# Kernel tuning notes

Hardware: AMD Instinct MI355X
Metric: run time of the kernel (lower is better)

The kernel has to match this reference:

```python
import jax, jax.numpy as jnp
import numpy as np

B, L, H, Z, T = 128, 4096, 1024, 256, 16  # batch, input_len(64*64), lstm_hidden, z_size, timesteps


def _lstm_cell(x, h, c, W_ih, b_ih, W_hh, b_hh):
    # PyTorch LSTMCell: gates ordered (input, forget, cell, output)
    gates = x @ W_ih.T + b_ih + h @ W_hh.T + b_hh
    i, f, g, o = jnp.split(gates, 4, axis=-1)
    c_new = jax.nn.sigmoid(f) * c + jax.nn.sigmoid(i) * jnp.tanh(g)
    h_new = jax.nn.sigmoid(o) * jnp.tanh(c_new)
    return h_new, c_new


def setup_inputs() -> dict:
    key = jax.random.key(0)
    ks = jax.random.split(key, 16)
    s = 0.02  # weight init scale
    return {
        "x": jax.random.uniform(ks[0], (B, L), dtype=jnp.float32),
        "eps": jax.random.normal(ks[1], (T, B, Z), dtype=jnp.float32),
        "c_0": jax.random.normal(ks[2], (1, L), dtype=jnp.float32),
        "h_0_enc": jax.random.normal(ks[3], (H,), dtype=jnp.float32),
        "h_0_dec": jax.random.normal(ks[4], (H,), dtype=jnp.float32),
        "W_ih_enc": jax.random.normal(ks[5], (4 * H, 2 * L + H), dtype=jnp.float32) * s,
        "b_ih_enc": jnp.zeros((4 * H,), dtype=jnp.float32),
        "W_hh_enc": jax.random.normal(ks[6], (4 * H, H), dtype=jnp.float32) * s,
        "b_hh_enc": jnp.zeros((4 * H,), dtype=jnp.float32),
        "W_mu": jax.random.normal(ks[7], (Z, H), dtype=jnp.float32) * s,
        "b_mu": jnp.zeros((Z,), dtype=jnp.float32),
        "W_sigma": jax.random.normal(ks[8], (Z, H), dtype=jnp.float32) * s,
        "b_sigma": jnp.zeros((Z,), dtype=jnp.float32),
        "W_ih_dec": jax.random.normal(ks[9], (4 * H, Z), dtype=jnp.float32) * s,
        "b_ih_dec": jnp.zeros((4 * H,), dtype=jnp.float32),
        "W_hh_dec": jax.random.normal(ks[10], (4 * H, H), dtype=jnp.float32) * s,
        "b_hh_dec": jnp.zeros((4 * H,), dtype=jnp.float32),
        "W_write": jax.random.normal(ks[11], (L, H), dtype=jnp.float32) * s,
        "b_write": jnp.zeros((L,), dtype=jnp.float32),
    }


def reference(x, eps, c_0, h_0_enc, h_0_dec,
              W_ih_enc, b_ih_enc, W_hh_enc, b_hh_enc,
              W_mu, b_mu, W_sigma, b_sigma,
              W_ih_dec, b_ih_dec, W_hh_dec, b_hh_dec,
              W_write, b_write):
    batch = x.shape[0]
    c_t = jnp.broadcast_to(c_0, (batch, L))
    h_enc = jnp.broadcast_to(h_0_enc, (batch, H))
    h_dec = jnp.broadcast_to(h_0_dec, (batch, H))
    c_enc = jnp.zeros((batch, H), dtype=x.dtype)
    c_dec = jnp.zeros((batch, H), dtype=x.dtype)

    def step(carry, eps_t):
        c_t, h_enc, c_enc, h_dec, c_dec = carry
        x_hat = x - jax.nn.sigmoid(c_t)
        r_t = jnp.concatenate((x, x_hat, h_dec), axis=-1)  # read + concat with h_dec
        h_enc, c_enc = _lstm_cell(r_t, h_enc, c_enc, W_ih_enc, b_ih_enc, W_hh_enc, b_hh_enc)
        mu = h_enc @ W_mu.T + b_mu
        logsigma = h_enc @ W_sigma.T + b_sigma
        z_t = eps_t * jnp.exp(logsigma) + mu
        h_dec, c_dec = _lstm_cell(z_t, h_dec, c_dec, W_ih_dec, b_ih_dec, W_hh_dec, b_hh_dec)
        c_t = c_t + h_dec @ W_write.T + b_write
        return (c_t, h_enc, c_enc, h_dec, c_dec), None

    (c_t, _, _, _, _), _ = jax.lax.scan(step, (c_t, h_enc, c_enc, h_dec, c_dec), eps)
    return jax.nn.sigmoid(c_t)
```

## Files before the change

### kernel.cpp

```cpp
#include <hip/hip_runtime.h>

#define B_   128
#define T_   16

typedef __bf16 bf16;
typedef __bf16 bf16x4 __attribute__((ext_vector_type(4)));
typedef __bf16 bf16x8 __attribute__((ext_vector_type(8)));
typedef float f32x4 __attribute__((ext_vector_type(4)));

#define GLL(SRC, DST) __builtin_amdgcn_global_load_lds( \
    (const __attribute__((address_space(1))) void*)(SRC), \
    (__attribute__((address_space(3))) void*)(DST), 16, 0, 0)

#define MFMA __builtin_amdgcn_mfma_f32_16x16x32_bf16
#define SLICE 524288

__device__ __forceinline__ float sigf(float x) { return 1.f / (1.f + expf(-x)); }

__device__ __forceinline__ void core64(
    bf16 (&As)[2][4096], bf16 (&Bs)[2][4096],
    const bf16* __restrict__ Ab, int lda,
    const bf16* __restrict__ Wb, int ldw,
    int nk, f32x4 (&acc)[4])
{
    const int tid = threadIdx.x, lane = tid & 63, wave = tid >> 6;
    const int srow = lane >> 3;
    const int scol = ((lane & 7) ^ srow) << 3;
    const int wr = wave & 1, wc = wave >> 1;
    const int ln = lane & 15;
    const int rA0 = wr * 32 + ln;
    const int rB0 = wc * 32 + ln;
    const int swz = (lane & 7) << 4;
    const int kq  = (lane >> 4) << 4;

    auto stage = [&](int b, int koff) {
        int c0 = wave, c1 = wave + 4;
        int ra0 = c0 * 8 + srow, ra1 = c1 * 8 + srow;
        GLL(Ab + (size_t)ra0 * lda + koff + scol, &As[b][c0 * 512]);
        GLL(Ab + (size_t)ra1 * lda + koff + scol, &As[b][c1 * 512]);
        GLL(Wb + (size_t)ra0 * ldw + koff + scol, &Bs[b][c0 * 512]);
        GLL(Wb + (size_t)ra1 * ldw + koff + scol, &Bs[b][c1 * 512]);
    };

    stage(0, 0);
    int bq = 0;
    for (int it = 0; it < nk; ++it) {
        __syncthreads();
        if (it + 1 < nk) stage(bq ^ 1, (it + 1) << 6);
        const bf16* as = As[bq];
        const bf16* bs = Bs[bq];
#pragma unroll
        for (int k2 = 0; k2 < 2; ++k2) {
            const int co = (((k2 << 6) | kq) ^ swz) >> 1;
            bf16x8 a0 = *(const bf16x8*)&as[rA0 * 64 + co];
            bf16x8 a1 = *(const bf16x8*)&as[(rA0 + 16) * 64 + co];
            bf16x8 b0 = *(const bf16x8*)&bs[rB0 * 64 + co];
            bf16x8 b1 = *(const bf16x8*)&bs[(rB0 + 16) * 64 + co];
            acc[0] = MFMA(a0, b0, acc[0], 0, 0, 0);
            acc[1] = MFMA(a0, b1, acc[1], 0, 0, 0);
            acc[2] = MFMA(a1, b0, acc[2], 0, 0, 0);
            acc[3] = MFMA(a1, b1, acc[3], 0, 0, 0);
        }
        bq ^= 1;
    }
}

__device__ __forceinline__ void store64f(float* __restrict__ P, int bm, int bn,
                                         f32x4 (&acc)[4])
{
    const int lane = threadIdx.x & 63, wave = threadIdx.x >> 6;
    const int wr = wave & 1, wc = wave >> 1;
    const int ln = lane & 15, q = lane >> 4;
    const int row0 = bm + wr * 32 + q * 4;
    const int col0 = bn + wc * 32 + ln;
#pragma unroll
    for (int r = 0; r < 4; ++r) {
        P[(size_t)(row0 + r) * 4096 + col0]           = acc[0][r];
        P[(size_t)(row0 + r) * 4096 + col0 + 16]      = acc[1][r];
        P[(size_t)(row0 + 16 + r) * 4096 + col0]      = acc[2][r];
        P[(size_t)(row0 + 16 + r) * 4096 + col0 + 16] = acc[3][r];
    }
}

__device__ __forceinline__ void store64b(bf16* __restrict__ P, int bm, int bn,
                                         f32x4 (&acc)[4])
{
    const int lane = threadIdx.x & 63, wave = threadIdx.x >> 6;
    const int wr = wave & 1, wc = wave >> 1;
    const int ln = lane & 15, q = lane >> 4;
    const int row0 = bm + wr * 32 + q * 4;
    const int col0 = bn + wc * 32 + ln;
#pragma unroll
    for (int r = 0; r < 4; ++r) {
        P[(size_t)(row0 + r) * 4096 + col0]           = (bf16)acc[0][r];
        P[(size_t)(row0 + r) * 4096 + col0 + 16]      = (bf16)acc[1][r];
        P[(size_t)(row0 + 16 + r) * 4096 + col0]      = (bf16)acc[2][r];
        P[(size_t)(row0 + 16 + r) * 4096 + col0 + 16] = (bf16)acc[3][r];
    }
}

__global__ __launch_bounds__(256) void gemm64_k(
    const bf16* __restrict__ A, int lda,
    const bf16* __restrict__ W, int ldw, int Kc,
    float* __restrict__ P)
{
    __shared__ bf16 As[2][4096], Bs[2][4096];
    const int nt = blockIdx.x, mt = blockIdx.y, zz = blockIdx.z;
    f32x4 acc[4];
#pragma unroll
    for (int i = 0; i < 4; ++i) acc[i] = (f32x4){0.f, 0.f, 0.f, 0.f};
    const bf16* Ab = A + (size_t)mt * 64 * lda + (size_t)zz * Kc;
    const bf16* Wb = W + (size_t)nt * 64 * ldw + (size_t)zz * Kc;
    core64(As, Bs, Ab, lda, Wb, ldw, Kc >> 6, acc);
    store64f(P + (size_t)zz * SLICE, mt * 64, nt * 64, acc);
}

__global__ __launch_bounds__(256) void gemm64b_k(
    const bf16* __restrict__ A, int lda,
    const bf16* __restrict__ W, int ldw, int Kc,
    bf16* __restrict__ P)
{
    __shared__ bf16 As[2][4096], Bs[2][4096];
    const int nt = blockIdx.x, mt = blockIdx.y, zz = blockIdx.z;
    f32x4 acc[4];
#pragma unroll
    for (int i = 0; i < 4; ++i) acc[i] = (f32x4){0.f, 0.f, 0.f, 0.f};
    const bf16* Ab = A + (size_t)mt * 64 * lda + (size_t)zz * Kc;
    const bf16* Wb = W + (size_t)nt * 64 * ldw + (size_t)zz * Kc;
    core64(As, Bs, Ab, lda, Wb, ldw, Kc >> 6, acc);
    store64b(P + (size_t)zz * SLICE, mt * 64, nt * 64, acc);
}

__global__ __launch_bounds__(256) void kE_k(
    const bf16* __restrict__ hh,   const bf16* __restrict__ Wwr,
    const bf16* __restrict__ Wcat, const bf16* __restrict__ Wdh,
    bf16* __restrict__ wrP, bf16* __restrict__ encP, bf16* __restrict__ decP,
    int zoff)
{
    __shared__ bf16 As[2][4096], Bs[2][4096];
    const int nt = blockIdx.x, mt = blockIdx.y, zz = blockIdx.z + zoff;
    f32x4 acc[4];
#pragma unroll
    for (int i = 0; i < 4; ++i) acc[i] = (f32x4){0.f, 0.f, 0.f, 0.f};

    const bf16* Ab;
    const bf16* Wb;
    int ldw;
    bf16* P;
    if (zz < 2) {
        Ab = hh + (size_t)mt * 64 * 2048 + zz * 512;
        Wb = Wwr + (size_t)nt * 64 * 1024 + zz * 512;
        ldw = 1024; P = wrP + (size_t)zz * SLICE;
    } else if (zz < 6) {
        int s = zz - 2;
        Ab = hh + (size_t)mt * 64 * 2048 + s * 512;
        Wb = Wcat + (size_t)nt * 64 * 2048 + s * 512;
        ldw = 2048; P = encP + (size_t)(8 + s) * SLICE;
    } else {
        int g = zz - 6;
        Ab = hh + (size_t)mt * 64 * 2048 + g * 512;
        Wb = Wdh + (size_t)nt * 64 * 1024 + g * 512;
        ldw = 1024; P = decP + (size_t)g * SLICE;
    }
    core64(As, Bs, Ab, 2048, Wb, ldw, 8, acc);
    store64b(P, mt * 64, nt * 64, acc);
}

__global__ __launch_bounds__(256) void fin0_k(
    const float* __restrict__ P, float* __restrict__ base,
    const float* __restrict__ b1, const float* __restrict__ b2)
{
    const int i = blockIdx.x * 256 + threadIdx.x;
    const int row = i >> 10, j = i & 1023;
    const size_t off = (size_t)row * 4096 + (j << 2);
    float s0 = 0.f, s1 = 0.f, s2 = 0.f, s3 = 0.f;
#pragma unroll
    for (int z = 0; z < 4; ++z) {
        float4 p = *(const float4*)(P + (size_t)z * SLICE + off);
        s0 += p.x; s1 += p.y; s2 += p.z; s3 += p.w;
    }
    base[off + 0] = s0 + b1[j]        + b2[j];
    base[off + 1] = s1 + b1[1024 + j] + b2[1024 + j];
    base[off + 2] = s2 + b1[2048 + j] + b2[2048 + j];
    base[off + 3] = s3 + b1[3072 + j] + b2[3072 + j];
}

__global__ __launch_bounds__(256) void kB_k(
    const bf16* __restrict__ encP, const float* __restrict__ base,
    float* __restrict__ c_enc, bf16* __restrict__ hh)
{
    const int i = blockIdx.x * 256 + threadIdx.x;
    const int row = i >> 10, j = i & 1023;
    const size_t off = (size_t)row * 4096 + (j << 2);
    float s0 = 0.f, s1 = 0.f, s2 = 0.f, s3 = 0.f;
#pragma unroll
    for (int z = 0; z < 12; ++z) {
        bf16x4 p = *(const bf16x4*)(encP + (size_t)z * SLICE + off);
        s0 += (float)p[0]; s1 += (float)p[1]; s2 += (float)p[2]; s3 += (float)p[3];
    }
    float4 bb = *(const float4*)(base + off);
    float gi = s0 + bb.x, gf = s1 + bb.y, gg = s2 + bb.z, go = s3 + bb.w;
    float cn = sigf(gf) * c_enc[i] + sigf(gi) * tanhf(gg);
    c_enc[i] = cn;
    hh[(size_t)row * 2048 + 1024 + j] = (bf16)(sigf(go) * tanhf(cn));
}

__global__ __launch_bounds__(256) void kF_k(
    const bf16* __restrict__ wrP, const float* __restrict__ b_wr,
    float* __restrict__ c_t, bf16* __restrict__ negs, float* __restrict__ outp)
{
    const int qi = blockIdx.x * 256 + threadIdx.x;
    const int row = qi >> 10, cq = qi & 1023;
    const size_t off = (size_t)row * 4096 + (cq << 2);
    bf16x4 p0 = *(const bf16x4*)(wrP + off);
    bf16x4 p1 = *(const bf16x4*)(wrP + SLICE + off);
    float4 cv = *(const float4*)(c_t + off);
    float4 bw = *(const float4*)(b_wr + (cq << 2));
    float v0 = cv.x + (float)p0[0] + (float)p1[0] + bw.x;
    float v1 = cv.y + (float)p0[1] + (float)p1[1] + bw.y;
    float v2 = cv.z + (float)p0[2] + (float)p1[2] + bw.z;
    float v3 = cv.w + (float)p0[3] + (float)p1[3] + bw.w;
    *(float4*)(c_t + off) = make_float4(v0, v1, v2, v3);
    negs[off + 0] = (bf16)(-sigf(v0));
    negs[off + 1] = (bf16)(-sigf(v1));
    negs[off + 2] = (bf16)(-sigf(v2));
    negs[off + 3] = (bf16)(-sigf(v3));
    if (outp)
        *(float4*)(outp + off) = make_float4(sigf(v0), sigf(v1), sigf(v2), sigf(v3));
}

struct SmemG32 {
    bf16 As[4][128][64];
    bf16 Ws[4][32][64];
};

__global__ __launch_bounds__(256) void kC_k(
    const bf16* __restrict__ hh, const bf16* __restrict__ Wms,
    const float* __restrict__ b_mu, const float* __restrict__ b_sig,
    const float* __restrict__ eps_t, bf16* __restrict__ zbf)
{
    __shared__ SmemG32 sm;
    const int nt = blockIdx.x;
    const int tid = threadIdx.x, lane = tid & 63, wave = tid >> 6;
    const int srow = lane >> 3, scol = ((lane & 7) ^ srow) << 3;
    const int ln = lane & 15, kq = (lane >> 4) << 4;
    const int swz = (lane & 7) << 4;
    const int rA = wave * 32 + ln;
    const bf16* Wb = Wms + (size_t)nt * 32 * 1024;
    const bf16* Ab = hh + 1024;

    f32x4 acc[2][2];
#pragma unroll
    for (int m = 0; m < 2; ++m)
#pragma unroll
        for (int n = 0; n < 2; ++n) acc[m][n] = (f32x4){0.f, 0.f, 0.f, 0.f};

    for (int it = 0; it < 4; ++it) {
        if (it) __syncthreads();
        const int koff = it * 256;
#pragma unroll
        for (int kc = 0; kc < 4; ++kc) {
            const int kg = koff + kc * 64 + scol;
#pragma unroll
            for (int i = 0; i < 4; ++i) {
                int rb = i * 32 + wave * 8;
                GLL(Ab + (size_t)(rb + srow) * 2048 + kg, &sm.As[kc][rb][0]);
            }
            GLL(Wb + (size_t)(wave * 8 + srow) * 1024 + kg, &sm.Ws[kc][wave * 8][0]);
        }
        __syncthreads();
#pragma unroll
        for (int kc = 0; kc < 4; ++kc)
#pragma unroll
            for (int k2 = 0; k2 < 2; ++k2) {
                const int co = (((k2 << 6) | kq) ^ swz) >> 1;
                bf16x8 a0 = *(const bf16x8*)&sm.As[kc][rA][co];
                bf16x8 a1 = *(const bf16x8*)&sm.As[kc][rA + 16][co];
                bf16x8 b0 = *(const bf16x8*)&sm.Ws[kc][ln][co];
                bf16x8 b1 = *(const bf16x8*)&sm.Ws[kc][ln + 16][co];
                acc[0][0] = MFMA(a0, b0, acc[0][0], 0, 0, 0);
                acc[0][1] = MFMA(a0, b1, acc[0][1], 0, 0, 0);
                acc[1][0] = MFMA(a1, b0, acc[1][0], 0, 0, 0);
                acc[1][1] = MFMA(a1, b1, acc[1][1], 0, 0, 0);
            }
    }
    __syncthreads();

    float* Cl = (float*)&sm;
    const int q = lane >> 4;
#pragma unroll
    for (int f = 0; f < 2; ++f)
#pragma unroll
        for (int n = 0; n < 2; ++n)
#pragma unroll
            for (int r = 0; r < 4; ++r)
                Cl[(wave * 32 + f * 16 + q * 4 + r) * 33 + n * 16 + ln] = acc[f][n][r];
    __syncthreads();

#pragma unroll
    for (int it = 0; it < 8; ++it) {
        int li = it * 256 + tid;
        int row = li >> 4, zl = li & 15;
        int zi = nt * 16 + zl;
        float mu = Cl[row * 33 + zl * 2]     + b_mu[zi];
        float ls = Cl[row * 33 + zl * 2 + 1] + b_sig[zi];
        float z = eps_t[row * 256 + zi] * expf(ls) + mu;
        zbf[(size_t)row * 256 + zi] = (bf16)z;
    }
}

struct SmemD {
    bf16 As[4][128][64];
    bf16 Ws[4][64][64];
};

__global__ __launch_bounds__(256) void kD_k(
    const bf16* __restrict__ zbf, const bf16* __restrict__ Wdz,
    const bf16* __restrict__ decP,
    const float* __restrict__ b_ihd, const float* __restrict__ b_hhd,
    float* __restrict__ c_dec, bf16* __restrict__ hh)
{
    __shared__ SmemD sm;
    const int nt = blockIdx.x;
    const int tid = threadIdx.x, lane = tid & 63, wave = tid >> 6;
    const int srow = lane >> 3, scol = ((lane & 7) ^ srow) << 3;
    const int ln = lane & 15, q = lane >> 4;
    const int kq = q << 4, swz = (lane & 7) << 4;
    const int wr = wave & 1, wc = wave >> 1;
    const bf16* Wb = Wdz + (size_t)nt * 64 * 256;

    f32x4 acc[4][2];
#pragma unroll
    for (int f = 0; f < 4; ++f)
#pragma unroll
        for (int n = 0; n < 2; ++n) acc[f][n] = (f32x4){0.f, 0.f, 0.f, 0.f};

#pragma unroll
    for (int kc = 0; kc < 4; ++kc) {
        const int kg = kc * 64 + scol;
#pragma unroll
        for (int i = 0; i < 4; ++i) {
            int rb = i * 32 + wave * 8;
            GLL(zbf + (size_t)(rb + srow) * 256 + kg, &sm.As[kc][rb][0]);
        }
#pragma unroll
        for (int i = 0; i < 2; ++i) {
            int rbw = i * 32 + wave * 8;
            GLL(Wb + (size_t)(rbw + srow) * 256 + kg, &sm.Ws[kc][rbw][0]);
        }
    }
    __syncthreads();
#pragma unroll
    for (int kc = 0; kc < 4; ++kc)
#pragma unroll
        for (int k2 = 0; k2 < 2; ++k2) {
            const int co = (((k2 << 6) | kq) ^ swz) >> 1;
            bf16x8 b0 = *(const bf16x8*)&sm.Ws[kc][wc * 32 + ln][co];
            bf16x8 b1 = *(const bf16x8*)&sm.Ws[kc][wc * 32 + ln + 16][co];
#pragma unroll
            for (int f = 0; f < 4; ++f) {
                bf16x8 a = *(const bf16x8*)&sm.As[kc][wr * 64 + f * 16 + ln][co];
                acc[f][0] = MFMA(a, b0, acc[f][0], 0, 0, 0);
                acc[f][1] = MFMA(a, b1, acc[f][1], 0, 0, 0);
            }
        }
    __syncthreads();

    float* Cl = (float*)&sm;
#pragma unroll
    for (int f = 0; f < 4; ++f)
#pragma unroll
        for (int n = 0; n < 2; ++n)
#pragma unroll
            for (int r = 0; r < 4; ++r)
                Cl[(wr * 64 + f * 16 + q * 4 + r) * 66 + wc * 32 + n * 16 + ln] = acc[f][n][r];
    __syncthreads();

#pragma unroll
    for (int it = 0; it < 8; ++it) {
        int li = it * 256 + tid;
        int row = li >> 4, jl = li & 15;
        int J = nt * 16 + jl;
        const float* cr = &Cl[row * 66 + jl * 4];
        int gcol = nt * 64 + jl * 4;
        const bf16* gp = decP + (size_t)row * 4096 + gcol;
        bf16x4 g0v = *(const bf16x4*)gp;
        bf16x4 g1v = *(const bf16x4*)(gp + SLICE);
        float gi = cr[0] + (float)g0v[0] + (float)g1v[0] + b_ihd[J]        + b_hhd[J];
        float gf = cr[1] + (float)g0v[1] + (float)g1v[1] + b_ihd[1024 + J] + b_hhd[1024 + J];
        float gg = cr[2] + (float)g0v[2] + (float)g1v[2] + b_ihd[2048 + J] + b_hhd[2048 + J];
        float go = cr[3] + (float)g0v[3] + (float)g1v[3] + b_ihd[3072 + J] + b_hhd[3072 + J];
        int ci = row * 1024 + J;
        float cn = sigf(gf) * c_dec[ci] + sigf(gi) * tanhf(gg);
        c_dec[ci] = cn;
        hh[(size_t)row * 2048 + J] = (bf16)(sigf(go) * tanhf(cn));
    }
}

#define PBL (B_ * 4096)
#define PBH (B_ * 1024)

__global__ void init_k(const float* __restrict__ x, const float* __restrict__ c0,
                       const float* __restrict__ h0e, const float* __restrict__ h0d,
                       float* __restrict__ c_t, float* __restrict__ c_enc,
                       float* __restrict__ c_dec, bf16* __restrict__ negs,
                       bf16* __restrict__ hh, bf16* __restrict__ x_bf) {
    int i = blockIdx.x * 256 + threadIdx.x;
    if (i >= PBL) return;
    int n = i & 4095;
    float c = c0[n];
    c_t[i] = c;
    negs[i] = (bf16)(-sigf(c));
    x_bf[i] = (bf16)x[i];
    if (i < PBH) {
        int row = i >> 10, j = i & 1023;
        c_enc[i] = 0.f;
        c_dec[i] = 0.f;
        hh[(size_t)row * 2048 + j]        = (bf16)h0d[j];
        hh[(size_t)row * 2048 + 1024 + j] = (bf16)h0e[j];
    }
}

__device__ __forceinline__ bf16x8 cvt8(const float* s) {
    float4 a = *(const float4*)s, b = *(const float4*)(s + 4);
    bf16x8 v = { (bf16)a.x, (bf16)a.y, (bf16)a.z, (bf16)a.w,
                 (bf16)b.x, (bf16)b.y, (bf16)b.z, (bf16)b.w };
    return v;
}

__global__ void conv_es_k(const float* __restrict__ Wih, const float* __restrict__ Whh,
                          bf16* __restrict__ wxh, bf16* __restrict__ wsum,
                          bf16* __restrict__ wcat) {
    int id = blockIdx.x * 256 + threadIdx.x;
    if (id >= 4096 * 768) return;
    int np = id / 768, c = (id - np * 768) * 8;
    int n = ((np & 3) << 10) + (np >> 2);
    if (c < 4096) {
        const float* sx = Wih + (size_t)n * 9216 + c;
        const float* sh = sx + 4096;
        float4 a = *(const float4*)sh, b = *(const float4*)(sh + 4);
        float4 e = *(const float4*)sx, f = *(const float4*)(sx + 4);
        bf16x8 vh = { (bf16)a.x, (bf16)a.y, (bf16)a.z, (bf16)a.w,
                      (bf16)b.x, (bf16)b.y, (bf16)b.z, (bf16)b.w };
        bf16x8 vs = { (bf16)(a.x + e.x), (bf16)(a.y + e.y), (bf16)(a.z + e.z), (bf16)(a.w + e.w),
                      (bf16)(b.x + f.x), (bf16)(b.y + f.y), (bf16)(b.z + f.z), (bf16)(b.w + f.w) };
        *(bf16x8*)(wxh  + (size_t)np * 4096 + c) = vh;
        *(bf16x8*)(wsum + (size_t)np * 4096 + c) = vs;
    } else if (c < 5120) {
        *(bf16x8*)(wcat + (size_t)np * 2048 + (c - 4096)) =
            cvt8(Wih + (size_t)n * 9216 + 8192 + (c - 4096));
    } else {
        *(bf16x8*)(wcat + (size_t)np * 2048 + 1024 + (c - 5120)) =
            cvt8(Whh + (size_t)n * 1024 + (c - 5120));
    }
}

__global__ void conv_dec_k(const float* __restrict__ Wih, const float* __restrict__ Whh,
                           bf16* __restrict__ wdz, bf16* __restrict__ wdh) {
    int id = blockIdx.x * 256 + threadIdx.x;
    if (id >= 4096 * 160) return;
    int np = id / 160, c = (id - np * 160) * 8;
    int n = ((np & 3) << 10) + (np >> 2);
    if (c < 256)
        *(bf16x8*)(wdz + (size_t)np * 256 + c) = cvt8(Wih + (size_t)n * 256 + c);
    else
        *(bf16x8*)(wdh + (size_t)np * 1024 + (c - 256)) =
            cvt8(Whh + (size_t)n * 1024 + (c - 256));
}

__global__ void conv_ms_k(const float* __restrict__ Wmu, const float* __restrict__ Wsig,
                          bf16* __restrict__ dst) {
    int id = blockIdx.x * 256 + threadIdx.x;
    if (id >= 512 * 128) return;
    int np = id >> 7, c = (id & 127) * 8;
    int zi = np >> 1;
    const float* src = ((np & 1) ? Wsig : Wmu) + (size_t)zi * 1024 + c;
    *(bf16x8*)(dst + (size_t)np * 1024 + c) = cvt8(src);
}

__global__ void conv_wr_k(const float* __restrict__ Wwr, bf16* __restrict__ dst) {
    int id = blockIdx.x * 256 + threadIdx.x;
    if (id >= 4096 * 128) return;
    *(bf16x8*)(dst + (size_t)id * 8) = cvt8(Wwr + (size_t)id * 8);
}

extern "C" void kernel_launch(void* const* d_in, const int* in_sizes, int n_in,
                              void* d_out, int out_size, void* d_ws, size_t ws_size,
                              hipStream_t stream) {
    const float* x      = (const float*)d_in[0];
    const float* eps    = (const float*)d_in[1];
    const float* c0     = (const float*)d_in[2];
    const float* h0e    = (const float*)d_in[3];
    const float* h0d    = (const float*)d_in[4];
    const float* W_ih_e = (const float*)d_in[5];
    const float* b_ih_e = (const float*)d_in[6];
    const float* W_hh_e = (const float*)d_in[7];
    const float* b_hh_e = (const float*)d_in[8];
    const float* W_mu   = (const float*)d_in[9];
    const float* b_mu   = (const float*)d_in[10];
    const float* W_sig  = (const float*)d_in[11];
    const float* b_sig  = (const float*)d_in[12];
    const float* W_ih_d = (const float*)d_in[13];
    const float* b_ih_d = (const float*)d_in[14];
    const float* W_hh_d = (const float*)d_in[15];
    const float* b_hh_d = (const float*)d_in[16];
    const float* W_wr   = (const float*)d_in[17];
    const float* b_wr   = (const float*)d_in[18];
    float* out = (float*)d_out;

    float* f = (float*)d_ws;
    float* c_t   = f; f += SLICE;
    float* base  = f; f += SLICE;
    float* pP    = f; f += (size_t)4 * SLICE;
    float* c_enc = f; f += 131072;
    float* c_dec = f; f += 131072;
    bf16* bp    = (bf16*)f;
    bf16* encP  = bp; bp += (size_t)12 * SLICE;
    bf16* decP  = bp; bp += (size_t)2 * SLICE;
    bf16* wrP   = bp; bp += (size_t)2 * SLICE;
    bf16* negs  = bp; bp += (size_t)B_ * 4096;
    bf16* hh    = bp; bp += (size_t)B_ * 2048;
    bf16* zbf   = bp; bp += (size_t)B_ * 256;
    bf16* x_bf  = bp; bp += (size_t)B_ * 4096;
    bf16* Wxh   = bp; bp += (size_t)4096 * 4096;
    bf16* Wsum  = bp; bp += (size_t)4096 * 4096;
    bf16* Wcat  = bp; bp += (size_t)4096 * 2048;
    bf16* Wdz   = bp; bp += (size_t)4096 * 256;
    bf16* Wdh   = bp; bp += (size_t)4096 * 1024;
    bf16* Wms   = bp; bp += (size_t)512 * 1024;
    bf16* Wwr   = bp; bp += (size_t)4096 * 1024;

    dim3 blk(256);

    init_k<<<(PBL + 255) / 256, blk, 0, stream>>>(x, c0, h0e, h0d, c_t, c_enc, c_dec,
                                                  negs, hh, x_bf);
    conv_es_k<<<(4096 * 768 + 255) / 256, blk, 0, stream>>>(W_ih_e, W_hh_e,
                                                            Wxh, Wsum, Wcat);
    conv_dec_k<<<(4096 * 160 + 255) / 256, blk, 0, stream>>>(W_ih_d, W_hh_d, Wdz, Wdh);
    conv_ms_k<<<(512 * 128 + 255) / 256, blk, 0, stream>>>(W_mu, W_sig, Wms);
    conv_wr_k<<<(4096 * 128 + 255) / 256, blk, 0, stream>>>(W_wr, Wwr);

    gemm64_k<<<dim3(64, 2, 4), blk, 0, stream>>>(x_bf, 4096, Wsum, 4096, 1024, pP);
    fin0_k<<<dim3(512), blk, 0, stream>>>(pP, base, b_ih_e, b_hh_e);

    kE_k<<<dim3(64, 2, 6), blk, 0, stream>>>(hh, Wwr, Wcat, Wdh, wrP, encP, decP, 2);

    for (int t = 0; t < T_; ++t) {
        gemm64b_k<<<dim3(64, 2, 8), blk, 0, stream>>>(negs, 4096, Wxh, 4096, 512, encP);
        kB_k<<<dim3(512), blk, 0, stream>>>(encP, base, c_enc, hh);
        kC_k<<<dim3(16), blk, 0, stream>>>(hh, Wms, b_mu, b_sig,
                                           eps + (size_t)t * (B_ * 256), zbf);
        kD_k<<<dim3(64), blk, 0, stream>>>(zbf, Wdz, decP, b_ih_d, b_hh_d, c_dec, hh);
        kE_k<<<dim3(64, 2, 8), blk, 0, stream>>>(hh, Wwr, Wcat, Wdh, wrP, encP, decP, 0);
        kF_k<<<dim3(512), blk, 0, stream>>>(wrP, b_wr, c_t, negs,
                                            (t == T_ - 1) ? out : nullptr);
    }
}
```

Measured before the change: 840.6 us.

## Merge prologue conversions, widen kB loads, and split kD across batch halves

Five separate weight-conversion and init kernels become one prolog kernel that dispatches on block index, which cuts launch overhead. kB now has each thread handle two hidden units with 16-byte bf16x8 loads over half as many blocks. kD is split into 128 blocks, each covering 64 batch rows, and reuses the shared core64 GEMM routine instead of its own custom load and MFMA loop. This raises parallelism in the small decoder GEMM but leaves each block with less work and possibly different pipelining.

```diff
diff --git a/kernel.cpp b/kernel.cpp
--- a/kernel.cpp
+++ b/kernel.cpp
@@ -190,19 +190,32 @@
     float* __restrict__ c_enc, bf16* __restrict__ hh)
 {
     const int i = blockIdx.x * 256 + threadIdx.x;
-    const int row = i >> 10, j = i & 1023;
-    const size_t off = (size_t)row * 4096 + (j << 2);
-    float s0 = 0.f, s1 = 0.f, s2 = 0.f, s3 = 0.f;
+    const int row = i >> 9, li = i & 511;
+    const size_t off = (size_t)row * 4096 + (li << 3);
+    float s[8] = {0.f, 0.f, 0.f, 0.f, 0.f, 0.f, 0.f, 0.f};
 #pragma unroll
     for (int z = 0; z < 12; ++z) {
-        bf16x4 p = *(const bf16x4*)(encP + (size_t)z * SLICE + off);
-        s0 += (float)p[0]; s1 += (float)p[1]; s2 += (float)p[2]; s3 += (float)p[3];
-    }
-    float4 bb = *(const float4*)(base + off);
-    float gi = s0 + bb.x, gf = s1 + bb.y, gg = s2 + bb.z, go = s3 + bb.w;
-    float cn = sigf(gf) * c_enc[i] + sigf(gi) * tanhf(gg);
-    c_enc[i] = cn;
-    hh[(size_t)row * 2048 + 1024 + j] = (bf16)(sigf(go) * tanhf(cn));
+        bf16x8 p = *(const bf16x8*)(encP + (size_t)z * SLICE + off);
+#pragma unroll
+        for (int k = 0; k < 8; ++k) s[k] += (float)p[k];
+    }
+    float4 bb0 = *(const float4*)(base + off);
+    float4 bb1 = *(const float4*)(base + off + 4);
+    const int j0 = li << 1;
+    {
+        float gi = s[0] + bb0.x, gf = s[1] + bb0.y, gg = s[2] + bb0.z, go = s[3] + bb0.w;
+        int ci = row * 1024 + j0;
+        float cn = sigf(gf) * c_enc[ci] + sigf(gi) * tanhf(gg);
+        c_enc[ci] = cn;
+        hh[(size_t)row * 2048 + 1024 + j0] = (bf16)(sigf(go) * tanhf(cn));
+    }
+    {
+        float gi = s[4] + bb1.x, gf = s[5] + bb1.y, gg = s[6] + bb1.z, go = s[7] + bb1.w;
+        int ci = row * 1024 + j0 + 1;
+        float cn = sigf(gf) * c_enc[ci] + sigf(gi) * tanhf(gg);
+        c_enc[ci] = cn;
+        hh[(size_t)row * 2048 + 1024 + j0 + 1] = (bf16)(sigf(go) * tanhf(cn));
+    }
 }
 
 __global__ __launch_bounds__(256) void kF_k(
@@ -309,10 +322,7 @@
     }
 }
 
-struct SmemD {
-    bf16 As[4][128][64];
-    bf16 Ws[4][64][64];
-};
+struct SmemK { bf16 A[2][4096]; bf16 B[2][4096]; };
 
 __global__ __launch_bounds__(256) void kD_k(
     const bf16* __restrict__ zbf, const bf16* __restrict__ Wdz,
@@ -320,70 +330,42 @@
     const float* __restrict__ b_ihd, const float* __restrict__ b_hhd,
     float* __restrict__ c_dec, bf16* __restrict__ hh)
 {
-    __shared__ SmemD sm;
-    const int nt = blockIdx.x;
+    __shared__ SmemK sm;
+    const int bid = blockIdx.x;
+    const int mt = bid & 1, nt = bid >> 1;
     const int tid = threadIdx.x, lane = tid & 63, wave = tid >> 6;
-    const int srow = lane >> 3, scol = ((lane & 7) ^ srow) << 3;
+    const int wr = wave & 1, wc = wave >> 1;
     const int ln = lane & 15, q = lane >> 4;
-    const int kq = q << 4, swz = (lane & 7) << 4;
-    const int wr = wave & 1, wc = wave >> 1;
+
+    const bf16* Ab = zbf + (size_t)mt * 64 * 256;
     const bf16* Wb = Wdz + (size_t)nt * 64 * 256;
-
-    f32x4 acc[4][2];
-#pragma unroll
-    for (int f = 0; f < 4; ++f)
-#pragma unroll
-        for (int n = 0; n < 2; ++n) acc[f][n] = (f32x4){0.f, 0.f, 0.f, 0.f};
-
-#pragma unroll
-    for (int kc = 0; kc < 4; ++kc) {
-        const int kg = kc * 64 + scol;
-#pragma unroll
-        for (int i = 0; i < 4; ++i) {
-            int rb = i * 32 + wave * 8;
-            GLL(zbf + (size_t)(rb + srow) * 256 + kg, &sm.As[kc][rb][0]);
-        }
-#pragma unroll
-        for (int i = 0; i < 2; ++i) {
-            int rbw = i * 32 + wave * 8;
-            GLL(Wb + (size_t)(rbw + srow) * 256 + kg, &sm.Ws[kc][rbw][0]);
-        }
-    }
+    f32x4 acc[4];
+#pragma unroll
+    for (int i = 0; i < 4; ++i) acc[i] = (f32x4){0.f, 0.f, 0.f, 0.f};
+    core64(sm.A, sm.B, Ab, 256, Wb, 256, 4, acc);
+
     __syncthreads();
-#pragma unroll
-    for (int kc = 0; kc < 4; ++kc)
-#pragma unroll
-        for (int k2 = 0; k2 < 2; ++k2) {
-            const int co = (((k2 << 6) | kq) ^ swz) >> 1;
-            bf16x8 b0 = *(const bf16x8*)&sm.Ws[kc][wc * 32 + ln][co];
-            bf16x8 b1 = *(const bf16x8*)&sm.Ws[kc][wc * 32 + ln + 16][co];
-#pragma unroll
-            for (int f = 0; f < 4; ++f) {
-                bf16x8 a = *(const bf16x8*)&sm.As[kc][wr * 64 + f * 16 + ln][co];
-                acc[f][0] = MFMA(a, b0, acc[f][0], 0, 0, 0);
-                acc[f][1] = MFMA(a, b1, acc[f][1], 0, 0, 0);
-            }
-        }
+    float* Cl = (float*)&sm;
+    const int r0 = wr * 32 + q * 4;
+    const int c0 = wc * 32 + ln;
+#pragma unroll
+    for (int r = 0; r < 4; ++r) {
+        Cl[(r0 + r) * 66 + c0]           = acc[0][r];
+        Cl[(r0 + r) * 66 + c0 + 16]      = acc[1][r];
+        Cl[(r0 + 16 + r) * 66 + c0]      = acc[2][r];
+        Cl[(r0 + 16 + r) * 66 + c0 + 16] = acc[3][r];
+    }
     __syncthreads();
 
-    float* Cl = (float*)&sm;
-#pragma unroll
-    for (int f = 0; f < 4; ++f)
-#pragma unroll
-        for (int n = 0; n < 2; ++n)
-#pragma unroll
-            for (int r = 0; r < 4; ++r)
-                Cl[(wr * 64 + f * 16 + q * 4 + r) * 66 + wc * 32 + n * 16 + ln] = acc[f][n][r];
-    __syncthreads();
-
-#pragma unroll
-    for (int it = 0; it < 8; ++it) {
+#pragma unroll
+    for (int it = 0; it < 4; ++it) {
         int li = it * 256 + tid;
-        int row = li >> 4, jl = li & 15;
-        int J = nt * 16 + jl;
-        const float* cr = &Cl[row * 66 + jl * 4];
-        int gcol = nt * 64 + jl * 4;
-        const bf16* gp = decP + (size_t)row * 4096 + gcol;
+        int lrow = li >> 4, jl = li & 15;
+        int row = mt * 64 + lrow;
+        int np0 = nt * 64 + jl * 4;
+        int J = np0 >> 2;
+        const float* cr = &Cl[lrow * 66 + jl * 4];
+        const bf16* gp = decP + (size_t)row * 4096 + np0;
         bf16x4 g0v = *(const bf16x4*)gp;
         bf16x4 g1v = *(const bf16x4*)(gp + SLICE);
         float gi = cr[0] + (float)g0v[0] + (float)g1v[0] + b_ihd[J]        + b_hhd[J];
@@ -400,13 +382,76 @@
 #define PBL (B_ * 4096)
 #define PBH (B_ * 1024)
 
-__global__ void init_k(const float* __restrict__ x, const float* __restrict__ c0,
-                       const float* __restrict__ h0e, const float* __restrict__ h0d,
-                       float* __restrict__ c_t, float* __restrict__ c_enc,
-                       float* __restrict__ c_dec, bf16* __restrict__ negs,
-                       bf16* __restrict__ hh, bf16* __restrict__ x_bf) {
-    int i = blockIdx.x * 256 + threadIdx.x;
-    if (i >= PBL) return;
+__device__ __forceinline__ bf16x8 cvt8(const float* s) {
+    float4 a = *(const float4*)s, b = *(const float4*)(s + 4);
+    bf16x8 v = { (bf16)a.x, (bf16)a.y, (bf16)a.z, (bf16)a.w,
+                 (bf16)b.x, (bf16)b.y, (bf16)b.z, (bf16)b.w };
+    return v;
+}
+
+__global__ __launch_bounds__(256) void prolog_k(
+    const float* __restrict__ x, const float* __restrict__ c0,
+    const float* __restrict__ h0e, const float* __restrict__ h0d,
+    const float* __restrict__ Wih_e, const float* __restrict__ Whh_e,
+    const float* __restrict__ Wih_d, const float* __restrict__ Whh_d,
+    const float* __restrict__ Wmu, const float* __restrict__ Wsig,
+    const float* __restrict__ Wwr_f,
+    float* __restrict__ c_t, float* __restrict__ c_enc, float* __restrict__ c_dec,
+    bf16* __restrict__ negs, bf16* __restrict__ hh, bf16* __restrict__ x_bf,
+    bf16* __restrict__ wxh, bf16* __restrict__ wsum, bf16* __restrict__ wcat,
+    bf16* __restrict__ wdz, bf16* __restrict__ wdh, bf16* __restrict__ wms,
+    bf16* __restrict__ wwr)
+{
+    const int bid = blockIdx.x;
+    if (bid < 12288) {
+        int id = bid * 256 + threadIdx.x;
+        int np = id / 768, c = (id - np * 768) * 8;
+        int n = ((np & 3) << 10) + (np >> 2);
+        if (c < 4096) {
+            const float* sx = Wih_e + (size_t)n * 9216 + c;
+            const float* sh = sx + 4096;
+            float4 a = *(const float4*)sh, b = *(const float4*)(sh + 4);
+            float4 e = *(const float4*)sx, f = *(const float4*)(sx + 4);
+            bf16x8 vh = { (bf16)a.x, (bf16)a.y, (bf16)a.z, (bf16)a.w,
+                          (bf16)b.x, (bf16)b.y, (bf16)b.z, (bf16)b.w };
+            bf16x8 vs = { (bf16)(a.x + e.x), (bf16)(a.y + e.y), (bf16)(a.z + e.z), (bf16)(a.w + e.w),
+                          (bf16)(b.x + f.x), (bf16)(b.y + f.y), (bf16)(b.z + f.z), (bf16)(b.w + f.w) };
+            *(bf16x8*)(wxh  + (size_t)np * 4096 + c) = vh;
+            *(bf16x8*)(wsum + (size_t)np * 4096 + c) = vs;
+        } else if (c < 5120) {
+            *(bf16x8*)(wcat + (size_t)np * 2048 + (c - 4096)) =
+                cvt8(Wih_e + (size_t)n * 9216 + 8192 + (c - 4096));
+        } else {
+            *(bf16x8*)(wcat + (size_t)np * 2048 + 1024 + (c - 5120)) =
+                cvt8(Whh_e + (size_t)n * 1024 + (c - 5120));
+        }
+        return;
+    }
+    if (bid < 12288 + 2560) {
+        int id = (bid - 12288) * 256 + threadIdx.x;
+        int np = id / 160, c = (id - np * 160) * 8;
+        int n = ((np & 3) << 10) + (np >> 2);
+        if (c < 256)
+            *(bf16x8*)(wdz + (size_t)np * 256 + c) = cvt8(Wih_d + (size_t)n * 256 + c);
+        else
+            *(bf16x8*)(wdh + (size_t)np * 1024 + (c - 256)) =
+                cvt8(Whh_d + (size_t)n * 1024 + (c - 256));
+        return;
+    }
+    if (bid < 12288 + 2560 + 256) {
+        int id = (bid - 12288 - 2560) * 256 + threadIdx.x;
+        int np = id >> 7, c = (id & 127) * 8;
+        int zi = np >> 1;
+        const float* src = ((np & 1) ? Wsig : Wmu) + (size_t)zi * 1024 + c;
+        *(bf16x8*)(wms + (size_t)np * 1024 + c) = cvt8(src);
+        return;
+    }
+    if (bid < 12288 + 2560 + 256 + 2048) {
+        int id = (bid - 12288 - 2560 - 256) * 256 + threadIdx.x;
+        *(bf16x8*)(wwr + (size_t)id * 8) = cvt8(Wwr_f + (size_t)id * 8);
+        return;
+    }
+    int i = (bid - 12288 - 2560 - 256 - 2048) * 256 + threadIdx.x;
     int n = i & 4095;
     float c = c0[n];
     c_t[i] = c;
@@ -419,69 +464,6 @@
         hh[(size_t)row * 2048 + j]        = (bf16)h0d[j];
         hh[(size_t)row * 2048 + 1024 + j] = (bf16)h0e[j];
     }
-}
-
-__device__ __forceinline__ bf16x8 cvt8(const float* s) {
-    float4 a = *(const float4*)s, b = *(const float4*)(s + 4);
-    bf16x8 v = { (bf16)a.x, (bf16)a.y, (bf16)a.z, (bf16)a.w,
-                 (bf16)b.x, (bf16)b.y, (bf16)b.z, (bf16)b.w };
-    return v;
-}
-
-__global__ void conv_es_k(const float* __restrict__ Wih, const float* __restrict__ Whh,
-                          bf16* __restrict__ wxh, bf16* __restrict__ wsum,
-                          bf16* __restrict__ wcat) {
-    int id = blockIdx.x * 256 + threadIdx.x;
-    if (id >= 4096 * 768) return;
-    int np = id / 768, c = (id - np * 768) * 8;
-    int n = ((np & 3) << 10) + (np >> 2);
-    if (c < 4096) {
-        const float* sx = Wih + (size_t)n * 9216 + c;
-        const float* sh = sx + 4096;
-        float4 a = *(const float4*)sh, b = *(const float4*)(sh + 4);
-        float4 e = *(const float4*)sx, f = *(const float4*)(sx + 4);
-        bf16x8 vh = { (bf16)a.x, (bf16)a.y, (bf16)a.z, (bf16)a.w,
-                      (bf16)b.x, (bf16)b.y, (bf16)b.z, (bf16)b.w };
-        bf16x8 vs = { (bf16)(a.x + e.x), (bf16)(a.y + e.y), (bf16)(a.z + e.z), (bf16)(a.w + e.w),
-                      (bf16)(b.x + f.x), (bf16)(b.y + f.y), (bf16)(b.z + f.z), (bf16)(b.w + f.w) };
-        *(bf16x8*)(wxh  + (size_t)np * 4096 + c) = vh;
-        *(bf16x8*)(wsum + (size_t)np * 4096 + c) = vs;
-    } else if (c < 5120) {
-        *(bf16x8*)(wcat + (size_t)np * 2048 + (c - 4096)) =
-            cvt8(Wih + (size_t)n * 9216 + 8192 + (c - 4096));
-    } else {
-        *(bf16x8*)(wcat + (size_t)np * 2048 + 1024 + (c - 5120)) =
-            cvt8(Whh + (size_t)n * 1024 + (c - 5120));
-    }
-}
-
-__global__ void conv_dec_k(const float* __restrict__ Wih, const float* __restrict__ Whh,
-                           bf16* __restrict__ wdz, bf16* __restrict__ wdh) {
-    int id = blockIdx.x * 256 + threadIdx.x;
-    if (id >= 4096 * 160) return;
-    int np = id / 160, c = (id - np * 160) * 8;
-    int n = ((np & 3) << 10) + (np >> 2);
-    if (c < 256)
-        *(bf16x8*)(wdz + (size_t)np * 256 + c) = cvt8(Wih + (size_t)n * 256 + c);
-    else
-        *(bf16x8*)(wdh + (size_t)np * 1024 + (c - 256)) =
-            cvt8(Whh + (size_t)n * 1024 + (c - 256));
-}
-
-__global__ void conv_ms_k(const float* __restrict__ Wmu, const float* __restrict__ Wsig,
-                          bf16* __restrict__ dst) {
-    int id = blockIdx.x * 256 + threadIdx.x;
-    if (id >= 512 * 128) return;
-    int np = id >> 7, c = (id & 127) * 8;
-    int zi = np >> 1;
-    const float* src = ((np & 1) ? Wsig : Wmu) + (size_t)zi * 1024 + c;
-    *(bf16x8*)(dst + (size_t)np * 1024 + c) = cvt8(src);
-}
-
-__global__ void conv_wr_k(const float* __restrict__ Wwr, bf16* __restrict__ dst) {
-    int id = blockIdx.x * 256 + threadIdx.x;
-    if (id >= 4096 * 128) return;
-    *(bf16x8*)(dst + (size_t)id * 8) = cvt8(Wwr + (size_t)id * 8);
 }
 
 extern "C" void kernel_launch(void* const* d_in, const int* in_sizes, int n_in,
@@ -532,13 +514,10 @@
 
     dim3 blk(256);
 
-    init_k<<<(PBL + 255) / 256, blk, 0, stream>>>(x, c0, h0e, h0d, c_t, c_enc, c_dec,
-                                                  negs, hh, x_bf);
-    conv_es_k<<<(4096 * 768 + 255) / 256, blk, 0, stream>>>(W_ih_e, W_hh_e,
-                                                            Wxh, Wsum, Wcat);
-    conv_dec_k<<<(4096 * 160 + 255) / 256, blk, 0, stream>>>(W_ih_d, W_hh_d, Wdz, Wdh);
-    conv_ms_k<<<(512 * 128 + 255) / 256, blk, 0, stream>>>(W_mu, W_sig, Wms);
-    conv_wr_k<<<(4096 * 128 + 255) / 256, blk, 0, stream>>>(W_wr, Wwr);
+    prolog_k<<<dim3(19200), blk, 0, stream>>>(
+        x, c0, h0e, h0d, W_ih_e, W_hh_e, W_ih_d, W_hh_d, W_mu, W_sig, W_wr,
+        c_t, c_enc, c_dec, negs, hh, x_bf,
+        Wxh, Wsum, Wcat, Wdz, Wdh, Wms, Wwr);
 
     gemm64_k<<<dim3(64, 2, 4), blk, 0, stream>>>(x_bf, 4096, Wsum, 4096, 1024, pP);
     fin0_k<<<dim3(512), blk, 0, stream>>>(pP, base, b_ih_e, b_hh_e);
@@ -547,10 +526,10 @@
 
     for (int t = 0; t < T_; ++t) {
         gemm64b_k<<<dim3(64, 2, 8), blk, 0, stream>>>(negs, 4096, Wxh, 4096, 512, encP);
-        kB_k<<<dim3(512), blk, 0, stream>>>(encP, base, c_enc, hh);
+        kB_k<<<dim3(256), blk, 0, stream>>>(encP, base, c_enc, hh);
         kC_k<<<dim3(16), blk, 0, stream>>>(hh, Wms, b_mu, b_sig,
                                            eps + (size_t)t * (B_ * 256), zbf);
-        kD_k<<<dim3(64), blk, 0, stream>>>(zbf, Wdz, decP, b_ih_d, b_hh_d, c_dec, hh);
+        kD_k<<<dim3(128), blk, 0, stream>>>(zbf, Wdz, decP, b_ih_d, b_hh_d, c_dec, hh);
         kE_k<<<dim3(64, 2, 8), blk, 0, stream>>>(hh, Wwr, Wcat, Wdh, wrP, encP, decP, 0);
         kF_k<<<dim3(512), blk, 0, stream>>>(wrP, b_wr, c_t, negs,
                                             (t == T_ - 1) ? out : nullptr);
```

Result: faster. 806.6 us (-4.0%).
